# Optimization experiments

Hardware: AMD Instinct MI355X
Metric: run time of the kernel (lower is better)

Reference implementation:

```python
import jax, jax.numpy as jnp
import numpy as np

N_QUBITS = 8
N_LAYERS = 7


def setup_inputs() -> dict:
    key = jax.random.key(0)
    ks = jax.random.split(key, 6)
    B = 65536
    return {
        "x": jax.random.normal(ks[0], (B, 2 ** N_QUBITS), dtype=jnp.float32),
        "weights": jax.random.normal(ks[1], (N_LAYERS, N_QUBITS), dtype=jnp.float32),
        "W1": jax.random.normal(ks[2], (16, 1), dtype=jnp.float32) * 0.5,
        "b1": jax.random.normal(ks[3], (16,), dtype=jnp.float32) * 0.1,
        "W2": jax.random.normal(ks[4], (1, 16), dtype=jnp.float32) * 0.5,
        "b2": jax.random.normal(ks[5], (1,), dtype=jnp.float32) * 0.1,
    }


def _apply_ry(psi, q, theta):
    # RY(theta) = [[cos(t/2), -sin(t/2)], [sin(t/2), cos(t/2)]] on wire q (axis q+1)
    c = jnp.cos(theta * 0.5)
    s = jnp.sin(theta * 0.5)
    a = jnp.take(psi, 0, axis=q + 1)
    b = jnp.take(psi, 1, axis=q + 1)
    return jnp.stack([c * a - s * b, s * a + c * b], axis=q + 1)


def _apply_cnot(psi, q):
    # CNOT control=q, target=q+1: flip target amplitudes where control=1
    ctl0 = jnp.take(psi, 0, axis=q + 1)
    ctl1 = jnp.take(psi, 1, axis=q + 1)
    # after removing axis q+1, target wire q+1 sits at axis q+1 of the slice
    ctl1 = jnp.flip(ctl1, axis=q + 1)
    return jnp.stack([ctl0, ctl1], axis=q + 1)


def _circuit(x, weights):
    B = x.shape[0]
    # AmplitudeEmbedding(normalize=True): real input -> real state (RY, CNOT are real)
    psi = x / jnp.linalg.norm(x, axis=1, keepdims=True)
    psi = psi.reshape((B,) + (2,) * N_QUBITS)  # axis 1 == wire 0 (MSB)
    for l in range(N_LAYERS):
        for q in range(N_QUBITS):
            psi = _apply_ry(psi, q, weights[l, q])
        for q in range(N_QUBITS - 1):
            psi = _apply_cnot(psi, q)
    probs = (psi ** 2).reshape(B, 2, -1)
    # <PauliZ(0)> = P(wire0=0) - P(wire0=1)
    return jnp.sum(probs[:, 0] - probs[:, 1], axis=1)


def reference(x, weights, W1, b1, W2, b2):
    z = _circuit(x, weights)[:, None]          # [B, 1]
    h = jax.nn.relu(z @ W1.T + b1)             # [B, 16]
    return jax.nn.sigmoid(h @ W2.T + b2)       # [B, 1]
```

## Files before the change

### kernel.cpp

```cpp
#include <hip/hip_runtime.h>
#include <hip/hip_bf16.h>

typedef __attribute__((ext_vector_type(8))) short bf16x8;
typedef __attribute__((ext_vector_type(4))) float f32x4;

__device__ __forceinline__ unsigned short f2bf(float f) {
    unsigned u = __builtin_bit_cast(unsigned, f);
    unsigned rnd = 0x7FFFu + ((u >> 16) & 1u);
    return (unsigned short)((u + rnd) >> 16);
}

__global__ __launch_bounds__(256) void qnn_setup(const float* __restrict__ wts,
                                                 unsigned short* __restrict__ Bp) {
    __shared__ float cs[56], sn[56];
    int tid = threadIdx.x;
    if (tid < 56) {
        float th = 0.5f * wts[tid];
        cs[tid] = cosf(th);
        sn[tid] = sinf(th);
    }
    __syncthreads();

    int l = tid & 63;
    int k = blockIdx.x * 4 + (tid >> 6);
    int a0 = l << 2;

    float v0 = (float)(a0 + 0 == k);
    float v1 = (float)(a0 + 1 == k);
    float v2 = (float)(a0 + 2 == k);
    float v3 = (float)(a0 + 3 == k);

#pragma unroll
    for (int L = 0; L < 7; ++L) {
#pragma unroll
        for (int q = 0; q <= 5; ++q) {
            int m = 5 - q;
            float c = cs[L * 8 + q], s = sn[L * 8 + q];
            float ss = ((l >> m) & 1) ? s : -s;
            float p0 = __shfl_xor(v0, 1 << m);
            float p1 = __shfl_xor(v1, 1 << m);
            float p2 = __shfl_xor(v2, 1 << m);
            float p3 = __shfl_xor(v3, 1 << m);
            v0 = fmaf(ss, p0, c * v0);
            v1 = fmaf(ss, p1, c * v1);
            v2 = fmaf(ss, p2, c * v2);
            v3 = fmaf(ss, p3, c * v3);
        }
        {
            float c = cs[L * 8 + 6], s = sn[L * 8 + 6];
            float n0 = fmaf(-s, v2, c * v0), n2 = fmaf(s, v0, c * v2);
            float n1 = fmaf(-s, v3, c * v1), n3 = fmaf(s, v1, c * v3);
            v0 = n0; v1 = n1; v2 = n2; v3 = n3;
        }
        {
            float c = cs[L * 8 + 7], s = sn[L * 8 + 7];
            float n0 = fmaf(-s, v1, c * v0), n1 = fmaf(s, v0, c * v1);
            float n2 = fmaf(-s, v3, c * v2), n3 = fmaf(s, v2, c * v3);
            v0 = n0; v1 = n1; v2 = n2; v3 = n3;
        }
        {
            int src = l;
#pragma unroll
            for (int q = 4; q >= 0; --q)
                src = src ^ (((src >> (5 - q)) & 1) << (4 - q));
            v0 = __shfl(v0, src);
            v1 = __shfl(v1, src);
            v2 = __shfl(v2, src);
            v3 = __shfl(v3, src);
        }
        {
            bool cc = (l & 1);
            float n0 = cc ? v2 : v0, n2 = cc ? v0 : v2;
            float n1 = cc ? v3 : v1, n3 = cc ? v1 : v3;
            v0 = n0; v1 = n1; v2 = n2; v3 = n3;
        }
        {
            float t = v2; v2 = v3; v3 = t;
        }
    }

    int t = k >> 5, j = k & 7, lk = (k >> 3) & 3;
#pragma unroll
    for (int r = 0; r < 4; ++r) {
        int n = a0 + r;
        int u = n >> 4;
        int ls = lk * 16 + (n & 15);
        float val = (r == 0) ? v0 : (r == 1) ? v1 : (r == 2) ? v2 : v3;
        Bp[(((u * 8 + t) * 64) + ls) * 8 + j] = f2bf(val);
    }
}

__global__ __launch_bounds__(512, 4) void qnn_main(
    const float* __restrict__ x, const unsigned short* __restrict__ Bp,
    const float* __restrict__ W1, const float* __restrict__ b1,
    const float* __restrict__ W2, const float* __restrict__ b2,
    float* __restrict__ out) {
    __shared__ __align__(16) unsigned short Xs[64][256];
    __shared__ float Qpart[8][64];
    __shared__ float Nrm[64];

    int tid = threadIdx.x;
    int l = tid & 63, w = tid >> 6;
    size_t base = (size_t)blockIdx.x * 64 * 256;

    const unsigned short* u0p = Bp + (size_t)(2 * w) * 4096 + l * 8;
    bf16x8 uf0[8], uf1[8];
#pragma unroll
    for (int t = 0; t < 8; ++t) {
        uf0[t] = *(const bf16x8*)(u0p + t * 512);
        uf1[t] = *(const bf16x8*)(u0p + 4096 + t * 512);
    }

    {
        int r = tid >> 3, qt = tid & 7;
        const float4* xr = (const float4*)(x + base + (size_t)r * 256 + qt * 32);
        float4 f[8];
#pragma unroll
        for (int i = 0; i < 8; ++i) f[i] = xr[i];
        float ssum = 0.f;
#pragma unroll
        for (int i = 0; i < 8; ++i) {
            float4 v = f[i];
            ssum = fmaf(v.x, v.x, fmaf(v.y, v.y, fmaf(v.z, v.z, fmaf(v.w, v.w, ssum))));
            ushort4 h;
            h.x = f2bf(v.x); h.y = f2bf(v.y); h.z = f2bf(v.z); h.w = f2bf(v.w);
            int col = qt * 32 + i * 4;
            int swz = (col >> 3) ^ (r & 7);
            *(ushort4*)&Xs[r][swz * 8 + (col & 7)] = h;
        }
        ssum += __shfl_xor(ssum, 1);
        ssum += __shfl_xor(ssum, 2);
        ssum += __shfl_xor(ssum, 4);
        if (qt == 0) Nrm[r] = ssum;
    }
    __syncthreads();

    int sl = l & 15, kg = l >> 4;
#pragma unroll
    for (int tau = 0; tau < 4; ++tau) {
        int srow = tau * 16 + sl;
        bf16x8 xf[8];
#pragma unroll
        for (int t = 0; t < 8; ++t)
            xf[t] = *(const bf16x8*)&Xs[srow][(((t << 2) + kg) ^ (srow & 7)) * 8];
        f32x4 a0 = {0.f, 0.f, 0.f, 0.f}, a1 = {0.f, 0.f, 0.f, 0.f};
#pragma unroll
        for (int t = 0; t < 8; ++t) {
            a0 = __builtin_amdgcn_mfma_f32_16x16x32_bf16(uf0[t], xf[t], a0, 0, 0, 0);
            a1 = __builtin_amdgcn_mfma_f32_16x16x32_bf16(uf1[t], xf[t], a1, 0, 0, 0);
        }
        float q = 0.f;
#pragma unroll
        for (int j = 0; j < 4; ++j)
            q = fmaf(a0[j], a0[j], fmaf(a1[j], a1[j], q));
        q += __shfl_xor(q, 16);
        q += __shfl_xor(q, 32);
        if (l < 16) Qpart[w][tau * 16 + l] = q;
    }
    __syncthreads();

    if (tid < 64) {
        float p = Qpart[0][tid] + Qpart[1][tid] + Qpart[2][tid] + Qpart[3][tid]
                - Qpart[4][tid] - Qpart[5][tid] - Qpart[6][tid] - Qpart[7][tid];
        float z = p / Nrm[tid];
        float o = b2[0];
#pragma unroll
        for (int jj = 0; jj < 16; ++jj) {
            float h = fmaf(z, W1[jj], b1[jj]);
            h = h > 0.f ? h : 0.f;
            o = fmaf(W2[jj], h, o);
        }
        out[(size_t)blockIdx.x * 64 + tid] = 1.f / (1.f + expf(-o));
    }
}

extern "C" void kernel_launch(void* const* d_in, const int* in_sizes, int n_in,
                              void* d_out, int out_size, void* d_ws, size_t ws_size,
                              hipStream_t stream) {
    const float* x   = (const float*)d_in[0];
    const float* wts = (const float*)d_in[1];
    const float* W1  = (const float*)d_in[2];
    const float* b1  = (const float*)d_in[3];
    const float* W2  = (const float*)d_in[4];
    const float* b2  = (const float*)d_in[5];
    float* out = (float*)d_out;
    unsigned short* Bp = (unsigned short*)d_ws;

    int B = in_sizes[0] >> 8;
    qnn_setup<<<64, 256, 0, stream>>>(wts, Bp);
    qnn_main<<<B / 64, 512, 0, stream>>>(x, Bp, W1, b1, W2, b2, out);
}
```

Baseline: 27.88 us.

## Pipeline x tiles with register prefetch and double-buffered LDS in persistent blocks

Each block now handles 256 rows instead of 64, split into eight 32-row tiles. Global loads for tile t+2 are issued into registers while the MFMA work runs on tile t, and the next tile is converted into an alternate LDS buffer. The goal is to hide HBM latency and amortize the per-block unitary fragment loads. In exchange the grid has 4x fewer blocks, occupancy is lowered to 2 blocks per CU, and a barrier is added per tile.

```diff
diff --git a/kernel.cpp b/kernel.cpp
--- a/kernel.cpp
+++ b/kernel.cpp
@@ -8,6 +8,13 @@
     unsigned u = __builtin_bit_cast(unsigned, f);
     unsigned rnd = 0x7FFFu + ((u >> 16) & 1u);
     return (unsigned short)((u + rnd) >> 16);
+}
+
+__device__ __forceinline__ void wg_barrier() {
+    asm volatile("s_waitcnt lgkmcnt(0)" ::: "memory");
+    __builtin_amdgcn_sched_barrier(0);
+    __builtin_amdgcn_s_barrier();
+    __builtin_amdgcn_sched_barrier(0);
 }
 
 __global__ __launch_bounds__(256) void qnn_setup(const float* __restrict__ wts,
@@ -90,18 +97,79 @@
     }
 }
 
-__global__ __launch_bounds__(512, 4) void qnn_main(
+__device__ __forceinline__ void issue_loads(const float* xb, float4 (&pf)[4]) {
+#pragma unroll
+    for (int i = 0; i < 4; ++i) pf[i] = *(const float4*)(xb + i * 4);
+}
+
+__device__ __forceinline__ void cvt_store(const float4 (&pf)[4],
+                                          unsigned short (*Xp)[256],
+                                          float* NrmRow, int sr, int qt) {
+    float ssum = 0.f;
+#pragma unroll
+    for (int i = 0; i < 4; ++i) {
+        float4 v = pf[i];
+        ssum = fmaf(v.x, v.x, fmaf(v.y, v.y, fmaf(v.z, v.z, fmaf(v.w, v.w, ssum))));
+        ushort4 h;
+        h.x = f2bf(v.x); h.y = f2bf(v.y); h.z = f2bf(v.z); h.w = f2bf(v.w);
+        int chunk = qt * 2 + (i >> 1);
+        int swz = chunk ^ (sr & 7);
+        *(ushort4*)&Xp[sr][swz * 8 + (i & 1) * 4] = h;
+    }
+    ssum += __shfl_xor(ssum, 1);
+    ssum += __shfl_xor(ssum, 2);
+    ssum += __shfl_xor(ssum, 4);
+    ssum += __shfl_xor(ssum, 8);
+    if (qt == 0) NrmRow[sr] = ssum;
+}
+
+__device__ __forceinline__ void compute_tile(const unsigned short (*Xp)[256],
+                                             const bf16x8 (&uf0)[8],
+                                             const bf16x8 (&uf1)[8],
+                                             float* QpRow, int l, int tbase) {
+    int sl = l & 15, kg = l >> 4;
+#pragma unroll
+    for (int tau = 0; tau < 2; ++tau) {
+        int srow = tau * 16 + sl;
+        bf16x8 xf[8];
+#pragma unroll
+        for (int t = 0; t < 8; ++t)
+            xf[t] = *(const bf16x8*)&Xp[srow][(((t << 2) + kg) ^ (srow & 7)) * 8];
+        f32x4 a0 = {0.f, 0.f, 0.f, 0.f}, a1 = {0.f, 0.f, 0.f, 0.f};
+#pragma unroll
+        for (int t = 0; t < 8; ++t) {
+            a0 = __builtin_amdgcn_mfma_f32_16x16x32_bf16(uf0[t], xf[t], a0, 0, 0, 0);
+            a1 = __builtin_amdgcn_mfma_f32_16x16x32_bf16(uf1[t], xf[t], a1, 0, 0, 0);
+        }
+        float q = 0.f;
+#pragma unroll
+        for (int j = 0; j < 4; ++j)
+            q = fmaf(a0[j], a0[j], fmaf(a1[j], a1[j], q));
+        q += __shfl_xor(q, 16);
+        q += __shfl_xor(q, 32);
+        if (l < 16) QpRow[tbase + tau * 16 + l] = q;
+    }
+}
+
+__global__ __launch_bounds__(512, 2) void qnn_main(
     const float* __restrict__ x, const unsigned short* __restrict__ Bp,
     const float* __restrict__ W1, const float* __restrict__ b1,
     const float* __restrict__ W2, const float* __restrict__ b2,
     float* __restrict__ out) {
-    __shared__ __align__(16) unsigned short Xs[64][256];
-    __shared__ float Qpart[8][64];
-    __shared__ float Nrm[64];
+    __shared__ __align__(16) unsigned short Xs[2][32][256];
+    __shared__ float Qpart[8][256];
+    __shared__ float Nrm[256];
 
     int tid = threadIdx.x;
     int l = tid & 63, w = tid >> 6;
-    size_t base = (size_t)blockIdx.x * 64 * 256;
+    int sr = tid >> 4, qt = tid & 15;
+    size_t base = (size_t)blockIdx.x * 256 * 256;
+
+    const float* xst = x + base + (size_t)sr * 256 + qt * 16;
+
+    float4 pf[2][4];
+    issue_loads(xst, pf[0]);
+    issue_loads(xst + 8192, pf[1]);
 
     const unsigned short* u0p = Bp + (size_t)(2 * w) * 4096 + l * 8;
     bf16x8 uf0[8], uf1[8];
@@ -111,55 +179,19 @@
         uf1[t] = *(const bf16x8*)(u0p + 4096 + t * 512);
     }
 
-    {
-        int r = tid >> 3, qt = tid & 7;
-        const float4* xr = (const float4*)(x + base + (size_t)r * 256 + qt * 32);
-        float4 f[8];
-#pragma unroll
-        for (int i = 0; i < 8; ++i) f[i] = xr[i];
-        float ssum = 0.f;
-#pragma unroll
-        for (int i = 0; i < 8; ++i) {
-            float4 v = f[i];
-            ssum = fmaf(v.x, v.x, fmaf(v.y, v.y, fmaf(v.z, v.z, fmaf(v.w, v.w, ssum))));
-            ushort4 h;
-            h.x = f2bf(v.x); h.y = f2bf(v.y); h.z = f2bf(v.z); h.w = f2bf(v.w);
-            int col = qt * 32 + i * 4;
-            int swz = (col >> 3) ^ (r & 7);
-            *(ushort4*)&Xs[r][swz * 8 + (col & 7)] = h;
-        }
-        ssum += __shfl_xor(ssum, 1);
-        ssum += __shfl_xor(ssum, 2);
-        ssum += __shfl_xor(ssum, 4);
-        if (qt == 0) Nrm[r] = ssum;
-    }
-    __syncthreads();
-
-    int sl = l & 15, kg = l >> 4;
-#pragma unroll
-    for (int tau = 0; tau < 4; ++tau) {
-        int srow = tau * 16 + sl;
-        bf16x8 xf[8];
-#pragma unroll
-        for (int t = 0; t < 8; ++t)
-            xf[t] = *(const bf16x8*)&Xs[srow][(((t << 2) + kg) ^ (srow & 7)) * 8];
-        f32x4 a0 = {0.f, 0.f, 0.f, 0.f}, a1 = {0.f, 0.f, 0.f, 0.f};
-#pragma unroll
-        for (int t = 0; t < 8; ++t) {
-            a0 = __builtin_amdgcn_mfma_f32_16x16x32_bf16(uf0[t], xf[t], a0, 0, 0, 0);
-            a1 = __builtin_amdgcn_mfma_f32_16x16x32_bf16(uf1[t], xf[t], a1, 0, 0, 0);
-        }
-        float q = 0.f;
-#pragma unroll
-        for (int j = 0; j < 4; ++j)
-            q = fmaf(a0[j], a0[j], fmaf(a1[j], a1[j], q));
-        q += __shfl_xor(q, 16);
-        q += __shfl_xor(q, 32);
-        if (l < 16) Qpart[w][tau * 16 + l] = q;
-    }
-    __syncthreads();
-
-    if (tid < 64) {
+    cvt_store(pf[0], Xs[0], Nrm, sr, qt);
+    wg_barrier();
+
+#pragma unroll
+    for (int t = 0; t < 8; ++t) {
+        if (t + 2 < 8) issue_loads(xst + (size_t)(t + 2) * 8192, pf[t & 1]);
+        compute_tile(Xs[t & 1], uf0, uf1, Qpart[w], l, t * 32);
+        if (t + 1 < 8)
+            cvt_store(pf[(t + 1) & 1], Xs[(t + 1) & 1], Nrm + (t + 1) * 32, sr, qt);
+        wg_barrier();
+    }
+
+    if (tid < 256) {
         float p = Qpart[0][tid] + Qpart[1][tid] + Qpart[2][tid] + Qpart[3][tid]
                 - Qpart[4][tid] - Qpart[5][tid] - Qpart[6][tid] - Qpart[7][tid];
         float z = p / Nrm[tid];
@@ -170,7 +202,7 @@
             h = h > 0.f ? h : 0.f;
             o = fmaf(W2[jj], h, o);
         }
-        out[(size_t)blockIdx.x * 64 + tid] = 1.f / (1.f + expf(-o));
+        out[(size_t)blockIdx.x * 256 + tid] = 1.f / (1.f + expf(-o));
     }
 }
 
@@ -188,5 +220,5 @@
 
     int B = in_sizes[0] >> 8;
     qnn_setup<<<64, 256, 0, stream>>>(wts, Bp);
-    qnn_main<<<B / 64, 512, 0, stream>>>(x, Bp, W1, b1, W2, b2, out);
-}
+    qnn_main<<<B / 256, 512, 0, stream>>>(x, Bp, W1, b1, W2, b2, out);
+}
```

Result: faster. 26.31 us (-5.6%).

## Stream x tiles into LDS via global_load_lds with double-buffered pipeline

Applied to the files above, without the earlier changes.

Rewrites the main kernel so each 256-thread block handles 128 rows in four 32-row tiles. Raw fp32 x is copied straight into padded LDS with global_load_lds, double-buffered, and the copies for later tiles overlap MFMA compute on earlier ones. Each wave now holds four U fragments, where it held two before, and does the bf16 conversion and norm accumulation while reading from LDS. The aim is to hide global load latency and skip the register-staging pass, at the cost of more registers per thread and more LDS per block, which lowers occupancy.

```diff
diff --git a/kernel.cpp b/kernel.cpp
--- a/kernel.cpp
+++ b/kernel.cpp
@@ -90,78 +90,114 @@
     }
 }
 
-__global__ __launch_bounds__(512, 4) void qnn_main(
+#define ROWF 260
+
+__device__ __forceinline__ void stage_tile(const float* __restrict__ xg,
+                                           float* dstbase, int w, int l) {
+#pragma unroll
+    for (int i = 0; i < 8; ++i) {
+        int r = w * 8 + i;
+        __builtin_amdgcn_global_load_lds(
+            (const __attribute__((address_space(1))) void*)
+                ((const char*)xg + (size_t)r * 1024 + l * 16),
+            (__attribute__((address_space(3))) void*)
+                ((char*)dstbase + r * 1040),
+            16, 0, 0);
+    }
+}
+
+__global__ __launch_bounds__(256, 2) void qnn_main(
     const float* __restrict__ x, const unsigned short* __restrict__ Bp,
     const float* __restrict__ W1, const float* __restrict__ b1,
     const float* __restrict__ W2, const float* __restrict__ b2,
     float* __restrict__ out) {
-    __shared__ __align__(16) unsigned short Xs[64][256];
-    __shared__ float Qpart[8][64];
-    __shared__ float Nrm[64];
+    __shared__ __align__(16) float XsF[2][32 * ROWF];
+    __shared__ float Qpart[4][128];
+    __shared__ float Nrm[128];
 
     int tid = threadIdx.x;
     int l = tid & 63, w = tid >> 6;
-    size_t base = (size_t)blockIdx.x * 64 * 256;
-
-    const unsigned short* u0p = Bp + (size_t)(2 * w) * 4096 + l * 8;
-    bf16x8 uf0[8], uf1[8];
+    size_t base = (size_t)blockIdx.x * 128 * 256;
+    const float* xb = x + base;
+
+    const unsigned short* up = Bp + (size_t)(4 * w) * 4096 + l * 8;
+    bf16x8 uf0[8], uf1[8], uf2[8], uf3[8];
 #pragma unroll
     for (int t = 0; t < 8; ++t) {
-        uf0[t] = *(const bf16x8*)(u0p + t * 512);
-        uf1[t] = *(const bf16x8*)(u0p + 4096 + t * 512);
-    }
-
-    {
-        int r = tid >> 3, qt = tid & 7;
-        const float4* xr = (const float4*)(x + base + (size_t)r * 256 + qt * 32);
-        float4 f[8];
-#pragma unroll
-        for (int i = 0; i < 8; ++i) f[i] = xr[i];
-        float ssum = 0.f;
-#pragma unroll
-        for (int i = 0; i < 8; ++i) {
-            float4 v = f[i];
-            ssum = fmaf(v.x, v.x, fmaf(v.y, v.y, fmaf(v.z, v.z, fmaf(v.w, v.w, ssum))));
-            ushort4 h;
-            h.x = f2bf(v.x); h.y = f2bf(v.y); h.z = f2bf(v.z); h.w = f2bf(v.w);
-            int col = qt * 32 + i * 4;
-            int swz = (col >> 3) ^ (r & 7);
-            *(ushort4*)&Xs[r][swz * 8 + (col & 7)] = h;
-        }
-        ssum += __shfl_xor(ssum, 1);
-        ssum += __shfl_xor(ssum, 2);
-        ssum += __shfl_xor(ssum, 4);
-        if (qt == 0) Nrm[r] = ssum;
-    }
+        uf0[t] = *(const bf16x8*)(up + t * 512);
+        uf1[t] = *(const bf16x8*)(up + 4096 + t * 512);
+        uf2[t] = *(const bf16x8*)(up + 8192 + t * 512);
+        uf3[t] = *(const bf16x8*)(up + 12288 + t * 512);
+    }
+    __builtin_amdgcn_sched_barrier(0);
+    stage_tile(xb, XsF[0], w, l);
+    __builtin_amdgcn_sched_barrier(0);
+    stage_tile(xb + 32 * 256, XsF[1], w, l);
+    __builtin_amdgcn_sched_barrier(0);
+    asm volatile("s_waitcnt vmcnt(8)" ::: "memory");
+    __builtin_amdgcn_sched_barrier(0);
+    __builtin_amdgcn_s_barrier();
+
+    int sl = l & 15, kg = l >> 4;
+
+#pragma unroll
+    for (int t = 0; t < 4; ++t) {
+        const float* buf = XsF[t & 1];
+#pragma unroll
+        for (int tau = 0; tau < 2; ++tau) {
+            const float* row = buf + (tau * 16 + sl) * ROWF + kg * 8;
+            f32x4 a0 = {0.f, 0.f, 0.f, 0.f}, a1 = {0.f, 0.f, 0.f, 0.f};
+            f32x4 a2 = {0.f, 0.f, 0.f, 0.f}, a3 = {0.f, 0.f, 0.f, 0.f};
+            float ss = 0.f;
+#pragma unroll
+            for (int ks = 0; ks < 8; ++ks) {
+                float4 f0 = *(const float4*)(row + ks * 32);
+                float4 f1 = *(const float4*)(row + ks * 32 + 4);
+                ss = fmaf(f0.x, f0.x, fmaf(f0.y, f0.y, fmaf(f0.z, f0.z, fmaf(f0.w, f0.w, ss))));
+                ss = fmaf(f1.x, f1.x, fmaf(f1.y, f1.y, fmaf(f1.z, f1.z, fmaf(f1.w, f1.w, ss))));
+                bf16x8 xf;
+                xf[0] = (short)f2bf(f0.x); xf[1] = (short)f2bf(f0.y);
+                xf[2] = (short)f2bf(f0.z); xf[3] = (short)f2bf(f0.w);
+                xf[4] = (short)f2bf(f1.x); xf[5] = (short)f2bf(f1.y);
+                xf[6] = (short)f2bf(f1.z); xf[7] = (short)f2bf(f1.w);
+                a0 = __builtin_amdgcn_mfma_f32_16x16x32_bf16(uf0[ks], xf, a0, 0, 0, 0);
+                a1 = __builtin_amdgcn_mfma_f32_16x16x32_bf16(uf1[ks], xf, a1, 0, 0, 0);
+                a2 = __builtin_amdgcn_mfma_f32_16x16x32_bf16(uf2[ks], xf, a2, 0, 0, 0);
+                a3 = __builtin_amdgcn_mfma_f32_16x16x32_bf16(uf3[ks], xf, a3, 0, 0, 0);
+            }
+            ss += __shfl_xor(ss, 16);
+            ss += __shfl_xor(ss, 32);
+            float q = 0.f;
+#pragma unroll
+            for (int j = 0; j < 4; ++j) {
+                q = fmaf(a0[j], a0[j], q);
+                q = fmaf(a1[j], a1[j], q);
+                q = fmaf(a2[j], a2[j], q);
+                q = fmaf(a3[j], a3[j], q);
+            }
+            q += __shfl_xor(q, 16);
+            q += __shfl_xor(q, 32);
+            if (l < 16) {
+                Qpart[w][t * 32 + tau * 16 + l] = q;
+                if (w == 0) Nrm[t * 32 + tau * 16 + l] = ss;
+            }
+        }
+        __builtin_amdgcn_s_barrier();
+        if (t < 2) {
+            stage_tile(xb + (size_t)(t + 2) * 32 * 256, XsF[t & 1], w, l);
+            __builtin_amdgcn_sched_barrier(0);
+        }
+        if (t < 3) {
+            if (t < 2) asm volatile("s_waitcnt vmcnt(8)" ::: "memory");
+            else       asm volatile("s_waitcnt vmcnt(0)" ::: "memory");
+            __builtin_amdgcn_sched_barrier(0);
+            __builtin_amdgcn_s_barrier();
+        }
+    }
+
     __syncthreads();
-
-    int sl = l & 15, kg = l >> 4;
-#pragma unroll
-    for (int tau = 0; tau < 4; ++tau) {
-        int srow = tau * 16 + sl;
-        bf16x8 xf[8];
-#pragma unroll
-        for (int t = 0; t < 8; ++t)
-            xf[t] = *(const bf16x8*)&Xs[srow][(((t << 2) + kg) ^ (srow & 7)) * 8];
-        f32x4 a0 = {0.f, 0.f, 0.f, 0.f}, a1 = {0.f, 0.f, 0.f, 0.f};
-#pragma unroll
-        for (int t = 0; t < 8; ++t) {
-            a0 = __builtin_amdgcn_mfma_f32_16x16x32_bf16(uf0[t], xf[t], a0, 0, 0, 0);
-            a1 = __builtin_amdgcn_mfma_f32_16x16x32_bf16(uf1[t], xf[t], a1, 0, 0, 0);
-        }
-        float q = 0.f;
-#pragma unroll
-        for (int j = 0; j < 4; ++j)
-            q = fmaf(a0[j], a0[j], fmaf(a1[j], a1[j], q));
-        q += __shfl_xor(q, 16);
-        q += __shfl_xor(q, 32);
-        if (l < 16) Qpart[w][tau * 16 + l] = q;
-    }
-    __syncthreads();
-
-    if (tid < 64) {
-        float p = Qpart[0][tid] + Qpart[1][tid] + Qpart[2][tid] + Qpart[3][tid]
-                - Qpart[4][tid] - Qpart[5][tid] - Qpart[6][tid] - Qpart[7][tid];
+    if (tid < 128) {
+        float p = Qpart[0][tid] + Qpart[1][tid] - Qpart[2][tid] - Qpart[3][tid];
         float z = p / Nrm[tid];
         float o = b2[0];
 #pragma unroll
@@ -170,7 +206,7 @@
             h = h > 0.f ? h : 0.f;
             o = fmaf(W2[jj], h, o);
         }
-        out[(size_t)blockIdx.x * 64 + tid] = 1.f / (1.f + expf(-o));
+        out[(size_t)blockIdx.x * 128 + tid] = 1.f / (1.f + expf(-o));
     }
 }
 
@@ -188,5 +224,5 @@
 
     int B = in_sizes[0] >> 8;
     qnn_setup<<<64, 256, 0, stream>>>(wts, Bp);
-    qnn_main<<<B / 64, 512, 0, stream>>>(x, Bp, W1, b1, W2, b2, out);
-}
+    qnn_main<<<B / 128, 256, 0, stream>>>(x, Bp, W1, b1, W2, b2, out);
+}
```

Result: slower. 30.59 us (+9.7%).

## Software-pipeline x loads with double-buffered LDS over 128-row blocks

Applied to the files above, without the earlier changes.

The main kernel now processes 128 rows per block in eight 16-row chunks. The next chunk's global loads are prefetched into registers while the current chunk runs its MFMAs, and a double-buffered LDS tile holds the converted bf16 data. This hides global load latency behind compute and halves the number of blocks, which amortises the per-block unitary fragment loads. The cost is a barrier per chunk, less memory parallelism per block, and half as many blocks in the grid.

```diff
diff --git a/kernel.cpp b/kernel.cpp
--- a/kernel.cpp
+++ b/kernel.cpp
@@ -8,6 +8,13 @@
     unsigned u = __builtin_bit_cast(unsigned, f);
     unsigned rnd = 0x7FFFu + ((u >> 16) & 1u);
     return (unsigned short)((u + rnd) >> 16);
+}
+
+__device__ __forceinline__ void wg_barrier() {
+    asm volatile("s_waitcnt lgkmcnt(0)" ::: "memory");
+    __builtin_amdgcn_sched_barrier(0);
+    __builtin_amdgcn_s_barrier();
+    __builtin_amdgcn_sched_barrier(0);
 }
 
 __global__ __launch_bounds__(256) void qnn_setup(const float* __restrict__ wts,
@@ -90,76 +97,88 @@
     }
 }
 
+__device__ __forceinline__ void cvt_store(const float4& a, const float4& b,
+                                          unsigned short (*Xp)[256],
+                                          float* NrmT, int sr, int qt) {
+    float ss = fmaf(a.x, a.x, fmaf(a.y, a.y, fmaf(a.z, a.z, a.w * a.w)));
+    ss = fmaf(b.x, b.x, fmaf(b.y, b.y, fmaf(b.z, b.z, fmaf(b.w, b.w, ss))));
+    bf16x8 h;
+    h[0] = (short)f2bf(a.x); h[1] = (short)f2bf(a.y);
+    h[2] = (short)f2bf(a.z); h[3] = (short)f2bf(a.w);
+    h[4] = (short)f2bf(b.x); h[5] = (short)f2bf(b.y);
+    h[6] = (short)f2bf(b.z); h[7] = (short)f2bf(b.w);
+    *(bf16x8*)&Xp[sr][(qt ^ (sr & 7)) * 8] = h;
+    ss += __shfl_xor(ss, 1);
+    ss += __shfl_xor(ss, 2);
+    ss += __shfl_xor(ss, 4);
+    ss += __shfl_xor(ss, 8);
+    ss += __shfl_xor(ss, 16);
+    if (qt == 0) NrmT[sr] = ss;
+}
+
 __global__ __launch_bounds__(512, 4) void qnn_main(
     const float* __restrict__ x, const unsigned short* __restrict__ Bp,
     const float* __restrict__ W1, const float* __restrict__ b1,
     const float* __restrict__ W2, const float* __restrict__ b2,
     float* __restrict__ out) {
-    __shared__ __align__(16) unsigned short Xs[64][256];
-    __shared__ float Qpart[8][64];
-    __shared__ float Nrm[64];
+    __shared__ __align__(16) unsigned short Xs[2][16][256];
+    __shared__ float Qpart[8][128];
+    __shared__ float Nrm[128];
 
     int tid = threadIdx.x;
     int l = tid & 63, w = tid >> 6;
-    size_t base = (size_t)blockIdx.x * 64 * 256;
-
-    const unsigned short* u0p = Bp + (size_t)(2 * w) * 4096 + l * 8;
+    int sr = tid >> 5, qt = tid & 31;
+    size_t base = (size_t)blockIdx.x * 128 * 256;
+    const float* xst = x + base + (size_t)sr * 256 + qt * 8;
+
+    const unsigned short* up = Bp + (size_t)(2 * w) * 4096 + l * 8;
     bf16x8 uf0[8], uf1[8];
 #pragma unroll
     for (int t = 0; t < 8; ++t) {
-        uf0[t] = *(const bf16x8*)(u0p + t * 512);
-        uf1[t] = *(const bf16x8*)(u0p + 4096 + t * 512);
-    }
-
-    {
-        int r = tid >> 3, qt = tid & 7;
-        const float4* xr = (const float4*)(x + base + (size_t)r * 256 + qt * 32);
-        float4 f[8];
-#pragma unroll
-        for (int i = 0; i < 8; ++i) f[i] = xr[i];
-        float ssum = 0.f;
-#pragma unroll
-        for (int i = 0; i < 8; ++i) {
-            float4 v = f[i];
-            ssum = fmaf(v.x, v.x, fmaf(v.y, v.y, fmaf(v.z, v.z, fmaf(v.w, v.w, ssum))));
-            ushort4 h;
-            h.x = f2bf(v.x); h.y = f2bf(v.y); h.z = f2bf(v.z); h.w = f2bf(v.w);
-            int col = qt * 32 + i * 4;
-            int swz = (col >> 3) ^ (r & 7);
-            *(ushort4*)&Xs[r][swz * 8 + (col & 7)] = h;
-        }
-        ssum += __shfl_xor(ssum, 1);
-        ssum += __shfl_xor(ssum, 2);
-        ssum += __shfl_xor(ssum, 4);
-        if (qt == 0) Nrm[r] = ssum;
-    }
-    __syncthreads();
-
-    int sl = l & 15, kg = l >> 4;
-#pragma unroll
-    for (int tau = 0; tau < 4; ++tau) {
-        int srow = tau * 16 + sl;
-        bf16x8 xf[8];
-#pragma unroll
-        for (int t = 0; t < 8; ++t)
-            xf[t] = *(const bf16x8*)&Xs[srow][(((t << 2) + kg) ^ (srow & 7)) * 8];
-        f32x4 a0 = {0.f, 0.f, 0.f, 0.f}, a1 = {0.f, 0.f, 0.f, 0.f};
-#pragma unroll
-        for (int t = 0; t < 8; ++t) {
-            a0 = __builtin_amdgcn_mfma_f32_16x16x32_bf16(uf0[t], xf[t], a0, 0, 0, 0);
-            a1 = __builtin_amdgcn_mfma_f32_16x16x32_bf16(uf1[t], xf[t], a1, 0, 0, 0);
-        }
-        float q = 0.f;
-#pragma unroll
-        for (int j = 0; j < 4; ++j)
-            q = fmaf(a0[j], a0[j], fmaf(a1[j], a1[j], q));
-        q += __shfl_xor(q, 16);
-        q += __shfl_xor(q, 32);
-        if (l < 16) Qpart[w][tau * 16 + l] = q;
-    }
-    __syncthreads();
-
-    if (tid < 64) {
+        uf0[t] = *(const bf16x8*)(up + t * 512);
+        uf1[t] = *(const bf16x8*)(up + 4096 + t * 512);
+    }
+
+    float4 pf[2][2];
+    pf[0][0] = *(const float4*)(xst);
+    pf[0][1] = *(const float4*)(xst + 4);
+    pf[1][0] = *(const float4*)(xst + 4096);
+    pf[1][1] = *(const float4*)(xst + 4100);
+    cvt_store(pf[0][0], pf[0][1], Xs[0], Nrm, sr, qt);
+    wg_barrier();
+
+    int row = l & 15, kg = l >> 4;
+
+#pragma unroll
+    for (int t = 0; t < 8; ++t) {
+        if (t + 2 < 8) {
+            pf[t & 1][0] = *(const float4*)(xst + (size_t)(t + 2) * 4096);
+            pf[t & 1][1] = *(const float4*)(xst + (size_t)(t + 2) * 4096 + 4);
+        }
+        {
+            const unsigned short* rp = &Xs[t & 1][row][0];
+            f32x4 a0 = {0.f, 0.f, 0.f, 0.f}, a1 = {0.f, 0.f, 0.f, 0.f};
+#pragma unroll
+            for (int ks = 0; ks < 8; ++ks) {
+                bf16x8 xf = *(const bf16x8*)(rp + (((ks << 2) | kg) ^ (row & 7)) * 8);
+                a0 = __builtin_amdgcn_mfma_f32_16x16x32_bf16(uf0[ks], xf, a0, 0, 0, 0);
+                a1 = __builtin_amdgcn_mfma_f32_16x16x32_bf16(uf1[ks], xf, a1, 0, 0, 0);
+            }
+            float q = 0.f;
+#pragma unroll
+            for (int j = 0; j < 4; ++j)
+                q = fmaf(a0[j], a0[j], fmaf(a1[j], a1[j], q));
+            q += __shfl_xor(q, 16);
+            q += __shfl_xor(q, 32);
+            if (l < 16) Qpart[w][t * 16 + l] = q;
+        }
+        if (t + 1 < 8)
+            cvt_store(pf[(t + 1) & 1][0], pf[(t + 1) & 1][1],
+                      Xs[(t + 1) & 1], Nrm + (t + 1) * 16, sr, qt);
+        wg_barrier();
+    }
+
+    if (tid < 128) {
         float p = Qpart[0][tid] + Qpart[1][tid] + Qpart[2][tid] + Qpart[3][tid]
                 - Qpart[4][tid] - Qpart[5][tid] - Qpart[6][tid] - Qpart[7][tid];
         float z = p / Nrm[tid];
@@ -170,7 +189,7 @@
             h = h > 0.f ? h : 0.f;
             o = fmaf(W2[jj], h, o);
         }
-        out[(size_t)blockIdx.x * 64 + tid] = 1.f / (1.f + expf(-o));
+        out[(size_t)blockIdx.x * 128 + tid] = 1.f / (1.f + expf(-o));
     }
 }
 
@@ -188,5 +207,5 @@
 
     int B = in_sizes[0] >> 8;
     qnn_setup<<<64, 256, 0, stream>>>(wts, Bp);
-    qnn_main<<<B / 64, 512, 0, stream>>>(x, Bp, W1, b1, W2, b2, out);
-}
+    qnn_main<<<B / 128, 512, 0, stream>>>(x, Bp, W1, b1, W2, b2, out);
+}
```

After: 23.91 us. 1.17x faster.
